# Optimization experiments

Measured on AMD Instinct MI355X. Metric: run time of the kernel, lower is better.

## Reference

```python
import jax, jax.numpy as jnp
import numpy as np

B, T, H, N = 4, 2048, 1024, 16
DT_MIN, DT_MAX = 1e-3, 1e-1
A_INIT_MIN, A_INIT_MAX = 0.5, 2.0


def _inv_softplus(x):
    # log(exp(x) - 1), numerically stable
    return x + jnp.log(-jnp.expm1(-x))


def setup_inputs() -> dict:
    key = jax.random.key(0)
    kx, ka, kb, kc, kw, kdt = jax.random.split(key, 6)
    x = jax.random.normal(kx, (B, T, H), dtype=jnp.float32)
    A_log = jax.random.uniform(ka, (H, N), minval=np.log(A_INIT_MIN), maxval=np.log(A_INIT_MAX), dtype=jnp.float32)
    B_mat = 0.02 * jax.random.normal(kb, (H, N), dtype=jnp.float32)
    C_mat = 0.02 * jax.random.normal(kc, (H, N), dtype=jnp.float32)
    D_vec = jnp.ones((H,), dtype=jnp.float32)
    W_dt = 0.02 * jax.random.normal(kw, (H, H), dtype=jnp.float32)
    b_dt = _inv_softplus(jax.random.uniform(kdt, (H,), minval=DT_MIN, maxval=DT_MAX, dtype=jnp.float32))
    return {"x": x, "A_log": A_log, "B_mat": B_mat, "C_mat": C_mat, "D_vec": D_vec, "W_dt": W_dt, "b_dt": b_dt}


def reference(x, A_log, B_mat, C_mat, D_vec, W_dt, b_dt):
    # in_proj is Identity since input_size == hidden_size
    u = x  # (B, T, H)
    A = -jnp.exp(A_log)  # (H, N)
    # dt for all timesteps at once: softplus(u @ W_dt^T + b_dt) -> (B, T, H)
    dt = jax.nn.softplus(jnp.einsum('bth,gh->btg', u, W_dt) + b_dt)
    state0 = jnp.zeros((u.shape[0], A_log.shape[0], A_log.shape[1]), dtype=u.dtype)

    def step(state, inp):
        dt_t, u_t = inp  # (B, H), (B, H)
        dtA = dt_t[..., None]  # (B, H, 1)
        A_bar = jnp.exp(dtA * A)                       # (B, H, N)
        state = A_bar * state + (dtA * B_mat) * u_t[..., None]
        y_t = jnp.einsum('bhn,hn->bh', state, C_mat) + D_vec * u_t
        return state, y_t

    # scan over time axis
    state_final, ys = jax.lax.scan(step, state0, (dt.transpose(1, 0, 2), u.transpose(1, 0, 2)))
    out = ys.transpose(1, 0, 2)  # (B, T, H)
    return out, state_final
```

## Files before the change

### kernel.cpp

```cpp
#include <hip/hip_runtime.h>
#include <stdint.h>

#define BB 4
#define TT 2048
#define HH 1024
#define NN 16
#define KK 1024
#define GG 1024
#define MM (BB*TT)
#define NCHUNK 16
#define TC (TT/NCHUNK)

#if __has_builtin(__builtin_amdgcn_exp2f)
#define FAST_EXP2(x) __builtin_amdgcn_exp2f(x)
#else
#define FAST_EXP2(x) __expf((x) * 0.6931471805599453f)
#endif
#define EXPSCALE 1.4426950408889634f

typedef __attribute__((ext_vector_type(8))) short short8;
typedef __attribute__((ext_vector_type(4))) float f32x4;

__device__ __forceinline__ unsigned short f2bf(float f) {
  union { float f; unsigned u; } a; a.f = f;
  unsigned u = a.u;
  u += 0x7fffu + ((u >> 16) & 1u);
  return (unsigned short)(u >> 16);
}

__global__ __launch_bounds__(256) void cvt_f32_bf16(const float* __restrict__ src,
                                                    unsigned short* __restrict__ dst, int n4) {
  int i = blockIdx.x * blockDim.x + threadIdx.x;
  if (i >= n4) return;
  float4 a = ((const float4*)src)[i];
  ushort4 o;
  o.x = f2bf(a.x); o.y = f2bf(a.y); o.z = f2bf(a.z); o.w = f2bf(a.w);
  ((ushort4*)dst)[i] = o;
}

__global__ __launch_bounds__(256) void gemm_dt(const unsigned short* __restrict__ xb,
                                               const unsigned short* __restrict__ wb,
                                               const float* __restrict__ b_dt,
                                               float* __restrict__ dtT) {
  __shared__ short lsA[128 * 32];
  __shared__ short lsB[64 * 32];
  const int tid  = threadIdx.x;
  const int w    = tid >> 6;
  const int lane = tid & 63;
  const int m0 = blockIdx.x * 128;
  const int g0 = blockIdx.y * 64;

  const int ea  = w * 1024 + lane * 8;
  const int am0 = ea >> 5,         ak0 = ea & 31;
  const int am1 = (ea + 512) >> 5, ak1 = (ea + 512) & 31;
  const int eb  = w * 512 + lane * 8;
  const int bg0 = eb >> 5,         bk0 = eb & 31;
  const unsigned short* gA0 = xb + (size_t)(m0 + am0) * KK + ak0;
  const unsigned short* gA1 = xb + (size_t)(m0 + am1) * KK + ak1;
  const unsigned short* gB0 = wb + (size_t)(g0 + bg0) * KK + bk0;
  short* lA0 = lsA + w * 1024;
  short* lB0 = lsB + w * 512;

  const int wm   = (w >> 1) * 64;
  const int wg   = (w & 1) * 32;
  const int lrow = lane & 15;
  const int lq   = lane >> 4;

  f32x4 acc[4][2];
  const f32x4 zero = {0.f, 0.f, 0.f, 0.f};
#pragma unroll
  for (int i = 0; i < 4; ++i)
#pragma unroll
    for (int j = 0; j < 2; ++j) acc[i][j] = zero;

  for (int kt = 0; kt < KK / 32; ++kt) {
    const int ko = kt * 32;
    __builtin_amdgcn_global_load_lds((__attribute__((address_space(1))) void*)(gA0 + ko),
                                     (__attribute__((address_space(3))) void*)(lA0), 16, 0, 0);
    __builtin_amdgcn_global_load_lds((__attribute__((address_space(1))) void*)(gA1 + ko),
                                     (__attribute__((address_space(3))) void*)(lA0 + 512), 16, 0, 0);
    __builtin_amdgcn_global_load_lds((__attribute__((address_space(1))) void*)(gB0 + ko),
                                     (__attribute__((address_space(3))) void*)(lB0), 16, 0, 0);
    __syncthreads();

    short8 af[4], bfr[2];
#pragma unroll
    for (int mi = 0; mi < 4; ++mi)
      af[mi] = *(const short8*)&lsA[(wm + mi * 16 + lrow) * 32 + lq * 8];
#pragma unroll
    for (int ni = 0; ni < 2; ++ni)
      bfr[ni] = *(const short8*)&lsB[(wg + ni * 16 + lrow) * 32 + lq * 8];
#pragma unroll
    for (int mi = 0; mi < 4; ++mi)
#pragma unroll
      for (int ni = 0; ni < 2; ++ni)
        acc[mi][ni] = __builtin_amdgcn_mfma_f32_16x16x32_bf16(af[mi], bfr[ni], acc[mi][ni], 0, 0, 0);
    __syncthreads();
  }

  const int b  = m0 >> 11;
  const int tb = (m0 & (TT - 1)) + wm + lq * 4;
#pragma unroll
  for (int mi = 0; mi < 4; ++mi)
#pragma unroll
    for (int ni = 0; ni < 2; ++ni) {
      const int gcol = g0 + wg + ni * 16 + lrow;
      const float bias = b_dt[gcol];
      f32x4 sp;
#pragma unroll
      for (int r = 0; r < 4; ++r) {
        float z = acc[mi][ni][r] + bias;
        sp[r] = fmaxf(z, 0.f) + __logf(1.f + __expf(-fabsf(z)));
      }
      *(f32x4*)&dtT[((size_t)b * HH + gcol) * TT + tb + mi * 16] = sp;
    }
}

__device__ __forceinline__ float reduce16(float (&v)[16], int n16) {
#pragma unroll
  for (int i = 0; i < 8; ++i) {
    float lo = v[i], hi = v[i + 8];
    float snd = (n16 & 8) ? lo : hi;
    float rcv = __shfl_xor(snd, 8);
    v[i] = ((n16 & 8) ? hi : lo) + rcv;
  }
#pragma unroll
  for (int i = 0; i < 4; ++i) {
    float lo = v[i], hi = v[i + 4];
    float snd = (n16 & 4) ? lo : hi;
    float rcv = __shfl_xor(snd, 4);
    v[i] = ((n16 & 4) ? hi : lo) + rcv;
  }
#pragma unroll
  for (int i = 0; i < 2; ++i) {
    float lo = v[i], hi = v[i + 2];
    float snd = (n16 & 2) ? lo : hi;
    float rcv = __shfl_xor(snd, 2);
    v[i] = ((n16 & 2) ? hi : lo) + rcv;
  }
  float lo = v[0], hi = v[1];
  float snd = (n16 & 1) ? lo : hi;
  float rcv = __shfl_xor(snd, 1);
  return ((n16 & 1) ? hi : lo) + rcv;
}

__device__ __forceinline__ float bcast16(float ureg, int idxbyte) {
  union { float f; int i; } a, r; a.f = ureg;
  r.i = __builtin_amdgcn_ds_bpermute(idxbyte, a.i);
  return r.f;
}

__device__ __forceinline__ void step16_p1(float& s, float& sd, const f32x4* dd, float ureg,
                                          int idxb, float Ae) {
#pragma unroll
  for (int q = 0; q < 4; ++q) {
#pragma unroll
    for (int k = 0; k < 4; ++k) {
      const int kk = q * 4 + k;
      float dtv = dd[q][k];
      float uv  = bcast16(ureg, idxb + kk * 4);
      float ab  = FAST_EXP2(dtv * Ae);
      s = fmaf(ab, s, dtv * uv);
      sd += dtv;
    }
  }
}

__device__ __forceinline__ void step16_p3(float& s, const f32x4* dd, float ureg, int idxb,
                                          float Ae, float Cb, float Dv,
                                          int n16, float* __restrict__ yp) {
  float v[16];
#pragma unroll
  for (int q = 0; q < 4; ++q) {
#pragma unroll
    for (int k = 0; k < 4; ++k) {
      const int kk = q * 4 + k;
      float dtv = dd[q][k];
      float uv  = bcast16(ureg, idxb + kk * 4);
      float ab  = FAST_EXP2(dtv * Ae);
      s = fmaf(ab, s, dtv * uv);
      v[kk] = Cb * s;
    }
  }
  float y = reduce16(v, n16);
  *yp = fmaf(Dv, ureg, y);
}

__global__ __launch_bounds__(256) void ssm_phase1(const float* __restrict__ x,
                                                  const float* __restrict__ dtT,
                                                  const float* __restrict__ A_log,
                                                  float* __restrict__ sloc,
                                                  float* __restrict__ decay) {
  const int tid = threadIdx.x;
  const int g   = tid >> 4;
  const int n16 = tid & 15;
  const int bid = blockIdx.x;
  const int ht  = bid & 63;
  const int b   = (bid >> 6) & 3;
  const int c   = bid >> 8;
  const int h   = (ht << 4) + g;
  const int lane = tid & 63;
  const int tl   = lane & 15;
  const int idxb = (lane & 48) << 2;

  const float Aneg = -__expf(A_log[h * NN + n16]);
  const float Ae   = Aneg * EXPSCALE;

  const f32x4* dp4 = (const f32x4*)(dtT + ((size_t)b * HH + h) * TT + c * TC);
  const float* up  = x + (size_t)b * TT * HH + (size_t)(c * TC + tl) * HH + h;

  float s = 0.f, sd = 0.f;
  f32x4 d0[4], d1[4];
  float u0, u1;
#pragma unroll
  for (int i = 0; i < 4; ++i) d0[i] = dp4[i];
  u0 = up[0];

#pragma unroll 1
  for (int j = 0; j < TC / 16; j += 2) {
#pragma unroll
    for (int i = 0; i < 4; ++i) d1[i] = dp4[(j + 1) * 4 + i];
    u1 = up[(size_t)(j + 1) * 16 * HH];
    step16_p1(s, sd, d0, u0, idxb, Ae);
    if (j + 2 < TC / 16) {
#pragma unroll
      for (int i = 0; i < 4; ++i) d0[i] = dp4[(j + 2) * 4 + i];
      u0 = up[(size_t)(j + 2) * 16 * HH];
    }
    step16_p1(s, sd, d1, u1, idxb, Ae);
  }

  const size_t idx = (((size_t)c * BB + b) * HH + h) * NN + n16;
  sloc[idx]  = s;
  decay[idx] = FAST_EXP2(Ae * sd);
}

__global__ __launch_bounds__(256) void ssm_phase2(float* __restrict__ sloc,
                                                  const float* __restrict__ decay,
                                                  const float* __restrict__ Bm_,
                                                  float* __restrict__ stateOut) {
  const int id = blockIdx.x * 256 + threadIdx.x;
  float carry = 0.f;
#pragma unroll
  for (int c = 0; c < NCHUNK; ++c) {
    const size_t idx = (size_t)c * (BB * HH * NN) + id;
    const float sl = sloc[idx];
    const float dc = decay[idx];
    sloc[idx] = carry;
    carry = fmaf(dc, carry, sl);
  }
  stateOut[id] = Bm_[id & (HH * NN - 1)] * carry;
}

__global__ __launch_bounds__(256) void ssm_phase3(const float* __restrict__ x,
                                                  const float* __restrict__ dtT,
                                                  const float* __restrict__ A_log,
                                                  const float* __restrict__ Bm_,
                                                  const float* __restrict__ Cm_,
                                                  const float* __restrict__ Dv_,
                                                  const float* __restrict__ carryBuf,
                                                  float* __restrict__ out) {
  const int tid = threadIdx.x;
  const int g   = tid >> 4;
  const int n16 = tid & 15;
  const int bid = blockIdx.x;
  const int ht  = bid & 63;
  const int b   = (bid >> 6) & 3;
  const int c   = bid >> 8;
  const int h   = (ht << 4) + g;
  const int lane = tid & 63;
  const int tl   = lane & 15;
  const int idxb = (lane & 48) << 2;

  const float Aneg = -__expf(A_log[h * NN + n16]);
  const float Ae   = Aneg * EXPSCALE;
  const float Cb   = Cm_[h * NN + n16] * Bm_[h * NN + n16];
  const float Dv   = Dv_[h];

  const f32x4* dp4 = (const f32x4*)(dtT + ((size_t)b * HH + h) * TT + c * TC);
  const float* up  = x + (size_t)b * TT * HH + (size_t)(c * TC + tl) * HH + h;
  float* yp = out + (size_t)b * TT * HH + (size_t)(c * TC + n16) * HH + h;

  float s = carryBuf[(((size_t)c * BB + b) * HH + h) * NN + n16];
  f32x4 d0[4], d1[4];
  float u0, u1;
#pragma unroll
  for (int i = 0; i < 4; ++i) d0[i] = dp4[i];
  u0 = up[0];

#pragma unroll 1
  for (int j = 0; j < TC / 16; j += 2) {
#pragma unroll
    for (int i = 0; i < 4; ++i) d1[i] = dp4[(j + 1) * 4 + i];
    u1 = up[(size_t)(j + 1) * 16 * HH];
    step16_p3(s, d0, u0, idxb, Ae, Cb, Dv, n16, yp);
    yp += 16 * HH;
    if (j + 2 < TC / 16) {
#pragma unroll
      for (int i = 0; i < 4; ++i) d0[i] = dp4[(j + 2) * 4 + i];
      u0 = up[(size_t)(j + 2) * 16 * HH];
    }
    step16_p3(s, d1, u1, idxb, Ae, Cb, Dv, n16, yp);
    yp += 16 * HH;
  }
}

extern "C" void kernel_launch(void* const* d_in, const int* in_sizes, int n_in,
                              void* d_out, int out_size, void* d_ws, size_t ws_size,
                              hipStream_t stream) {
  const float* x     = (const float*)d_in[0];
  const float* A_log = (const float*)d_in[1];
  const float* B_mat = (const float*)d_in[2];
  const float* C_mat = (const float*)d_in[3];
  const float* D_vec = (const float*)d_in[4];
  const float* W_dt  = (const float*)d_in[5];
  const float* b_dt  = (const float*)d_in[6];
  float* out = (float*)d_out;

  char* ws = (char*)d_ws;
  unsigned short* xb  = (unsigned short*)(ws);
  unsigned short* wb  = (unsigned short*)(ws + 16777216);
  float*          dtT = (float*)(ws + 18874368);
  float*          sloc  = (float*)(ws);
  float*          decay = (float*)(ws + 4194304);
  float* stateOut = out + (size_t)BB * TT * HH;

  cvt_f32_bf16<<<(MM * KK / 4 + 255) / 256, 256, 0, stream>>>(x, xb, MM * KK / 4);
  cvt_f32_bf16<<<(GG * KK / 4 + 255) / 256, 256, 0, stream>>>(W_dt, wb, GG * KK / 4);
  gemm_dt<<<dim3(MM / 128, GG / 64), 256, 0, stream>>>(xb, wb, b_dt, dtT);

  const int nblk = BB * (HH / 16) * NCHUNK;
  ssm_phase1<<<nblk, 256, 0, stream>>>(x, dtT, A_log, sloc, decay);
  ssm_phase2<<<(BB * HH * NN) / 256, 256, 0, stream>>>(sloc, decay, B_mat, stateOut);
  ssm_phase3<<<nblk, 256, 0, stream>>>(x, dtT, A_log, B_mat, C_mat, D_vec, sloc, out);
}
```

Before: 208.4 us.

## Map one thread per channel with all 16 states in registers, finer chunks

Rewrites the chunked scan phases so each thread owns one hidden channel and keeps all 16 state entries in registers. This replaces the per-(h,n) thread mapping, which needed ds_bpermute broadcasts and a shuffle reduction for the output. Inputs for a chunk are staged in shared memory, and chunk count grows from 16 to 64 to restore parallelism. Phase 2 now stores only the summed dt per chunk and recomputes decay, which cuts workspace traffic. The cost is higher register pressure, more chunks for the serial carry pass, and sloc writes that quadruple.

```diff
diff --git a/kernel.cpp b/kernel.cpp
--- a/kernel.cpp
+++ b/kernel.cpp
@@ -8,8 +8,9 @@
 #define KK 1024
 #define GG 1024
 #define MM (BB*TT)
-#define NCHUNK 16
+#define NCHUNK 64
 #define TC (TT/NCHUNK)
+#define HB 256
 
 #if __has_builtin(__builtin_amdgcn_exp2f)
 #define FAST_EXP2(x) __builtin_amdgcn_exp2f(x)
@@ -116,192 +117,154 @@
     }
 }
 
-__device__ __forceinline__ float reduce16(float (&v)[16], int n16) {
+__global__ __launch_bounds__(256, 4) void ssm_phase1(const float* __restrict__ x,
+                                                     const float* __restrict__ dtT,
+                                                     const float* __restrict__ A_log,
+                                                     float* __restrict__ sloc,
+                                                     float* __restrict__ sdArr) {
+  __shared__ float uT[TC][HB];
+  const int tid = threadIdx.x;
+  const int bid = blockIdx.x;
+  const int hb = bid & (HH / HB - 1);
+  const int b  = (bid >> 2) & (BB - 1);
+  const int c  = bid >> 4;
+  const int h  = hb * HB + tid;
+
+  const float* xg = x + (size_t)b * TT * HH + (size_t)c * TC * HH + hb * HB;
 #pragma unroll
   for (int i = 0; i < 8; ++i) {
-    float lo = v[i], hi = v[i + 8];
-    float snd = (n16 & 8) ? lo : hi;
-    float rcv = __shfl_xor(snd, 8);
-    v[i] = ((n16 & 8) ? hi : lo) + rcv;
-  }
-#pragma unroll
-  for (int i = 0; i < 4; ++i) {
-    float lo = v[i], hi = v[i + 4];
-    float snd = (n16 & 4) ? lo : hi;
-    float rcv = __shfl_xor(snd, 4);
-    v[i] = ((n16 & 4) ? hi : lo) + rcv;
-  }
-#pragma unroll
-  for (int i = 0; i < 2; ++i) {
-    float lo = v[i], hi = v[i + 2];
-    float snd = (n16 & 2) ? lo : hi;
-    float rcv = __shfl_xor(snd, 2);
-    v[i] = ((n16 & 2) ? hi : lo) + rcv;
-  }
-  float lo = v[0], hi = v[1];
-  float snd = (n16 & 1) ? lo : hi;
-  float rcv = __shfl_xor(snd, 1);
-  return ((n16 & 1) ? hi : lo) + rcv;
-}
-
-__device__ __forceinline__ float bcast16(float ureg, int idxbyte) {
-  union { float f; int i; } a, r; a.f = ureg;
-  r.i = __builtin_amdgcn_ds_bpermute(idxbyte, a.i);
-  return r.f;
-}
-
-__device__ __forceinline__ void step16_p1(float& s, float& sd, const f32x4* dd, float ureg,
-                                          int idxb, float Ae) {
-#pragma unroll
-  for (int q = 0; q < 4; ++q) {
+    const int t   = i * 4 + (tid >> 6);
+    const int col = (tid & 63) * 4;
+    *(f32x4*)&uT[t][col] = *(const f32x4*)&xg[(size_t)t * HH + col];
+  }
+
+  const float* dp = dtT + ((size_t)b * HH + h) * TT + c * TC;
+  f32x4 dd[8];
+#pragma unroll
+  for (int i = 0; i < 8; ++i) dd[i] = ((const f32x4*)dp)[i];
+
+  float Ae[NN];
+#pragma unroll
+  for (int n = 0; n < NN; ++n) Ae[n] = -__expf(A_log[h * NN + n]) * EXPSCALE;
+
+  float s[NN];
+#pragma unroll
+  for (int n = 0; n < NN; ++n) s[n] = 0.f;
+  float sd = 0.f;
+
+  __syncthreads();
+
+#pragma unroll
+  for (int jt = 0; jt < 8; ++jt) {
 #pragma unroll
     for (int k = 0; k < 4; ++k) {
-      const int kk = q * 4 + k;
-      float dtv = dd[q][k];
-      float uv  = bcast16(ureg, idxb + kk * 4);
-      float ab  = FAST_EXP2(dtv * Ae);
-      s = fmaf(ab, s, dtv * uv);
+      const int t = jt * 4 + k;
+      const float dtv = dd[jt][k];
+      const float du  = dtv * uT[t][tid];
       sd += dtv;
+#pragma unroll
+      for (int n = 0; n < NN; ++n) {
+        const float ab = FAST_EXP2(dtv * Ae[n]);
+        s[n] = fmaf(ab, s[n], du);
+      }
     }
   }
-}
-
-__device__ __forceinline__ void step16_p3(float& s, const f32x4* dd, float ureg, int idxb,
-                                          float Ae, float Cb, float Dv,
-                                          int n16, float* __restrict__ yp) {
-  float v[16];
-#pragma unroll
-  for (int q = 0; q < 4; ++q) {
-#pragma unroll
-    for (int k = 0; k < 4; ++k) {
-      const int kk = q * 4 + k;
-      float dtv = dd[q][k];
-      float uv  = bcast16(ureg, idxb + kk * 4);
-      float ab  = FAST_EXP2(dtv * Ae);
-      s = fmaf(ab, s, dtv * uv);
-      v[kk] = Cb * s;
-    }
-  }
-  float y = reduce16(v, n16);
-  *yp = fmaf(Dv, ureg, y);
-}
-
-__global__ __launch_bounds__(256) void ssm_phase1(const float* __restrict__ x,
-                                                  const float* __restrict__ dtT,
+
+  float* sp = sloc + (((size_t)c * BB + b) * HH + h) * NN;
+#pragma unroll
+  for (int n = 0; n < NN; n += 4) {
+    f32x4 v = {s[n], s[n + 1], s[n + 2], s[n + 3]};
+    *(f32x4*)&sp[n] = v;
+  }
+  sdArr[((size_t)c * BB + b) * HH + h] = sd;
+}
+
+__global__ __launch_bounds__(256) void ssm_phase2(float* __restrict__ sloc,
+                                                  const float* __restrict__ sdArr,
                                                   const float* __restrict__ A_log,
-                                                  float* __restrict__ sloc,
-                                                  float* __restrict__ decay) {
-  const int tid = threadIdx.x;
-  const int g   = tid >> 4;
-  const int n16 = tid & 15;
-  const int bid = blockIdx.x;
-  const int ht  = bid & 63;
-  const int b   = (bid >> 6) & 3;
-  const int c   = bid >> 8;
-  const int h   = (ht << 4) + g;
-  const int lane = tid & 63;
-  const int tl   = lane & 15;
-  const int idxb = (lane & 48) << 2;
-
-  const float Aneg = -__expf(A_log[h * NN + n16]);
-  const float Ae   = Aneg * EXPSCALE;
-
-  const f32x4* dp4 = (const f32x4*)(dtT + ((size_t)b * HH + h) * TT + c * TC);
-  const float* up  = x + (size_t)b * TT * HH + (size_t)(c * TC + tl) * HH + h;
-
-  float s = 0.f, sd = 0.f;
-  f32x4 d0[4], d1[4];
-  float u0, u1;
-#pragma unroll
-  for (int i = 0; i < 4; ++i) d0[i] = dp4[i];
-  u0 = up[0];
-
-#pragma unroll 1
-  for (int j = 0; j < TC / 16; j += 2) {
-#pragma unroll
-    for (int i = 0; i < 4; ++i) d1[i] = dp4[(j + 1) * 4 + i];
-    u1 = up[(size_t)(j + 1) * 16 * HH];
-    step16_p1(s, sd, d0, u0, idxb, Ae);
-    if (j + 2 < TC / 16) {
-#pragma unroll
-      for (int i = 0; i < 4; ++i) d0[i] = dp4[(j + 2) * 4 + i];
-      u0 = up[(size_t)(j + 2) * 16 * HH];
-    }
-    step16_p1(s, sd, d1, u1, idxb, Ae);
-  }
-
-  const size_t idx = (((size_t)c * BB + b) * HH + h) * NN + n16;
-  sloc[idx]  = s;
-  decay[idx] = FAST_EXP2(Ae * sd);
-}
-
-__global__ __launch_bounds__(256) void ssm_phase2(float* __restrict__ sloc,
-                                                  const float* __restrict__ decay,
                                                   const float* __restrict__ Bm_,
                                                   float* __restrict__ stateOut) {
   const int id = blockIdx.x * 256 + threadIdx.x;
+  const int hn = id & (HH * NN - 1);
+  const int bh = id >> 4;
+  const float Ae = -__expf(A_log[hn]) * EXPSCALE;
   float carry = 0.f;
-#pragma unroll
-  for (int c = 0; c < NCHUNK; ++c) {
-    const size_t idx = (size_t)c * (BB * HH * NN) + id;
+  for (int ch = 0; ch < NCHUNK; ++ch) {
+    const size_t idx = (size_t)ch * (BB * HH * NN) + id;
     const float sl = sloc[idx];
-    const float dc = decay[idx];
+    const float dc = FAST_EXP2(Ae * sdArr[(size_t)ch * (BB * HH) + bh]);
     sloc[idx] = carry;
     carry = fmaf(dc, carry, sl);
   }
-  stateOut[id] = Bm_[id & (HH * NN - 1)] * carry;
-}
-
-__global__ __launch_bounds__(256) void ssm_phase3(const float* __restrict__ x,
-                                                  const float* __restrict__ dtT,
-                                                  const float* __restrict__ A_log,
-                                                  const float* __restrict__ Bm_,
-                                                  const float* __restrict__ Cm_,
-                                                  const float* __restrict__ Dv_,
-                                                  const float* __restrict__ carryBuf,
-                                                  float* __restrict__ out) {
+  stateOut[id] = Bm_[hn] * carry;
+}
+
+__global__ __launch_bounds__(256, 4) void ssm_phase3(const float* __restrict__ x,
+                                                     const float* __restrict__ dtT,
+                                                     const float* __restrict__ A_log,
+                                                     const float* __restrict__ Bm_,
+                                                     const float* __restrict__ Cm_,
+                                                     const float* __restrict__ Dv_,
+                                                     const float* __restrict__ carryBuf,
+                                                     float* __restrict__ out) {
+  __shared__ float uT[TC][HB];
   const int tid = threadIdx.x;
-  const int g   = tid >> 4;
-  const int n16 = tid & 15;
   const int bid = blockIdx.x;
-  const int ht  = bid & 63;
-  const int b   = (bid >> 6) & 3;
-  const int c   = bid >> 8;
-  const int h   = (ht << 4) + g;
-  const int lane = tid & 63;
-  const int tl   = lane & 15;
-  const int idxb = (lane & 48) << 2;
-
-  const float Aneg = -__expf(A_log[h * NN + n16]);
-  const float Ae   = Aneg * EXPSCALE;
-  const float Cb   = Cm_[h * NN + n16] * Bm_[h * NN + n16];
-  const float Dv   = Dv_[h];
-
-  const f32x4* dp4 = (const f32x4*)(dtT + ((size_t)b * HH + h) * TT + c * TC);
-  const float* up  = x + (size_t)b * TT * HH + (size_t)(c * TC + tl) * HH + h;
-  float* yp = out + (size_t)b * TT * HH + (size_t)(c * TC + n16) * HH + h;
-
-  float s = carryBuf[(((size_t)c * BB + b) * HH + h) * NN + n16];
-  f32x4 d0[4], d1[4];
-  float u0, u1;
-#pragma unroll
-  for (int i = 0; i < 4; ++i) d0[i] = dp4[i];
-  u0 = up[0];
-
-#pragma unroll 1
-  for (int j = 0; j < TC / 16; j += 2) {
-#pragma unroll
-    for (int i = 0; i < 4; ++i) d1[i] = dp4[(j + 1) * 4 + i];
-    u1 = up[(size_t)(j + 1) * 16 * HH];
-    step16_p3(s, d0, u0, idxb, Ae, Cb, Dv, n16, yp);
-    yp += 16 * HH;
-    if (j + 2 < TC / 16) {
-#pragma unroll
-      for (int i = 0; i < 4; ++i) d0[i] = dp4[(j + 2) * 4 + i];
-      u0 = up[(size_t)(j + 2) * 16 * HH];
+  const int hb = bid & (HH / HB - 1);
+  const int b  = (bid >> 2) & (BB - 1);
+  const int c  = bid >> 4;
+  const int h  = hb * HB + tid;
+
+  const float* xg = x + (size_t)b * TT * HH + (size_t)c * TC * HH + hb * HB;
+#pragma unroll
+  for (int i = 0; i < 8; ++i) {
+    const int t   = i * 4 + (tid >> 6);
+    const int col = (tid & 63) * 4;
+    *(f32x4*)&uT[t][col] = *(const f32x4*)&xg[(size_t)t * HH + col];
+  }
+
+  const float* dp = dtT + ((size_t)b * HH + h) * TT + c * TC;
+  f32x4 dd[8];
+#pragma unroll
+  for (int i = 0; i < 8; ++i) dd[i] = ((const f32x4*)dp)[i];
+
+  float Ae[NN], Cb[NN];
+#pragma unroll
+  for (int n = 0; n < NN; ++n) {
+    Ae[n] = -__expf(A_log[h * NN + n]) * EXPSCALE;
+    Cb[n] = Cm_[h * NN + n] * Bm_[h * NN + n];
+  }
+  const float Dv = Dv_[h];
+
+  float s[NN];
+  const float* cp = carryBuf + (((size_t)c * BB + b) * HH + h) * NN;
+#pragma unroll
+  for (int n = 0; n < NN; n += 4) {
+    f32x4 v = *(const f32x4*)&cp[n];
+    s[n] = v[0]; s[n + 1] = v[1]; s[n + 2] = v[2]; s[n + 3] = v[3];
+  }
+
+  float* yo = out + (size_t)b * TT * HH + (size_t)c * TC * HH + h;
+
+  __syncthreads();
+
+#pragma unroll
+  for (int jt = 0; jt < 8; ++jt) {
+#pragma unroll
+    for (int k = 0; k < 4; ++k) {
+      const int t = jt * 4 + k;
+      const float dtv = dd[jt][k];
+      const float uv  = uT[t][tid];
+      const float du  = dtv * uv;
+      float y = Dv * uv;
+#pragma unroll
+      for (int n = 0; n < NN; ++n) {
+        const float ab = FAST_EXP2(dtv * Ae[n]);
+        s[n] = fmaf(ab, s[n], du);
+        y = fmaf(Cb[n], s[n], y);
+      }
+      yo[(size_t)t * HH] = y;
     }
-    step16_p3(s, d1, u1, idxb, Ae, Cb, Dv, n16, yp);
-    yp += 16 * HH;
   }
 }
 
@@ -322,15 +285,15 @@
   unsigned short* wb  = (unsigned short*)(ws + 16777216);
   float*          dtT = (float*)(ws + 18874368);
   float*          sloc  = (float*)(ws);
-  float*          decay = (float*)(ws + 4194304);
+  float*          sdArr = (float*)(ws + 16777216);
   float* stateOut = out + (size_t)BB * TT * HH;
 
   cvt_f32_bf16<<<(MM * KK / 4 + 255) / 256, 256, 0, stream>>>(x, xb, MM * KK / 4);
   cvt_f32_bf16<<<(GG * KK / 4 + 255) / 256, 256, 0, stream>>>(W_dt, wb, GG * KK / 4);
   gemm_dt<<<dim3(MM / 128, GG / 64), 256, 0, stream>>>(xb, wb, b_dt, dtT);
 
-  const int nblk = BB * (HH / 16) * NCHUNK;
-  ssm_phase1<<<nblk, 256, 0, stream>>>(x, dtT, A_log, sloc, decay);
-  ssm_phase2<<<(BB * HH * NN) / 256, 256, 0, stream>>>(sloc, decay, B_mat, stateOut);
+  const int nblk = (HH / HB) * BB * NCHUNK;
+  ssm_phase1<<<nblk, 256, 0, stream>>>(x, dtT, A_log, sloc, sdArr);
+  ssm_phase2<<<(BB * HH * NN) / 256, 256, 0, stream>>>(sloc, sdArr, A_log, B_mat, stateOut);
   ssm_phase3<<<nblk, 256, 0, stream>>>(x, dtT, A_log, B_mat, C_mat, D_vec, sloc, out);
 }
```

Measured after the change: 184.9 us. 1.13x faster.
